# Optimization experiments

Hardware: AMD Instinct MI355X
Metric: run time of the kernel (lower is better)

## Reference

```python
import jax, jax.numpy as jnp
import numpy as np
import math

B, N, L = 1, 256, 384
D_MSA, D_PAIR, H, DH = 256, 128, 8, 32


def layer_norm(x, g, b, eps=1e-5):
    m = jnp.mean(x, axis=-1, keepdims=True)
    v = jnp.var(x, axis=-1, keepdims=True)
    return (x - m) * jax.lax.rsqrt(v + eps) * g + b


def setup_inputs() -> dict:
    key = jax.random.key(0)
    ks = jax.random.split(key, 16)
    hd = H * DH
    w = lambda k, shp, s=0.05: (jax.random.normal(k, shp, dtype=jnp.float32) * s)
    return {
        "msa": jax.random.normal(ks[0], (B, N, L, D_MSA), dtype=jnp.float32),
        "pair": jax.random.normal(ks[1], (B, L, L, D_PAIR), dtype=jnp.float32),
        "ln_msa_g": jnp.ones((D_MSA,), jnp.float32),
        "ln_msa_b": jnp.zeros((D_MSA,), jnp.float32),
        "ln_pair_g": jnp.ones((D_PAIR,), jnp.float32),
        "ln_pair_b": jnp.zeros((D_PAIR,), jnp.float32),
        "sw_q_w": w(ks[2], (D_MSA, hd)),
        "sw_q_b": jnp.zeros((hd,), jnp.float32),
        "sw_k_w": w(ks[3], (D_MSA, hd)),
        "sw_k_b": jnp.zeros((hd,), jnp.float32),
        "wq": w(ks[4], (D_MSA, hd)),
        "wk": w(ks[5], (D_MSA, hd)),
        "wv": w(ks[6], (D_MSA, hd)),
        "wb": w(ks[7], (D_PAIR, H)),
        "wg": w(ks[8], (D_MSA, hd)),
        "bg": jnp.ones((hd,), jnp.float32),
        "wo": w(ks[9], (hd, D_MSA)),
        "bo": jnp.zeros((D_MSA,), jnp.float32),
    }


def reference(msa, pair, ln_msa_g, ln_msa_b, ln_pair_g, ln_pair_b,
              sw_q_w, sw_q_b, sw_k_w, sw_k_b,
              wq, wk, wv, wb, wg, bg, wo, bo):
    b, n, l, _ = msa.shape
    scale = 1.0 / math.sqrt(DH)

    msa_n = layer_norm(msa, ln_msa_g, ln_msa_b)
    pair_n = layer_norm(pair, ln_pair_g, ln_pair_b)

    # SequenceWeight: attention of target seq (row 0) over all N rows, per (L, head)
    tar = msa_n[:, 0]                                       # [B,L,D]
    swq = (tar @ sw_q_w + sw_q_b).reshape(b, l, H, DH) * scale
    swk = (msa_n @ sw_k_w + sw_k_b).reshape(b, n, l, H, DH)
    sw_logits = jnp.einsum('blhd,bnlhd->bnlh', swq, swk)    # [B,N,L,H]
    seq_weight = jax.nn.softmax(sw_logits, axis=1)          # softmax over N (dropout: eval)

    query = (msa_n @ wq).reshape(b, n, l, H, DH) * seq_weight[..., None]
    key = (msa_n @ wk).reshape(b, n, l, H, DH) * scale
    value = (msa_n @ wv).reshape(b, n, l, H, DH)
    bias = pair_n @ wb                                      # [B,L,L,H]
    gate = jax.nn.sigmoid(msa_n @ wg + bg)                  # [B,N,L,H*DH]

    attn = jnp.einsum('bsqhd,bskhd->bqkh', query, key) + bias
    attn = jax.nn.softmax(attn, axis=-2)                    # over k axis
    out = jnp.einsum('bqkh,bskhd->bsqhd', attn, value).reshape(b, n, l, H * DH)
    out = gate * out
    return out @ wo + bo
```

## Files before the change

kernel.cpp:

```cpp
#include <hip/hip_runtime.h>
#include <hip/hip_fp16.h>
#include <stdint.h>

#define NSEQ 256
#define LSEQ 384
#define DM   256
#define DP   128
#define NH   8
#define DHD  32
#define NL   (NSEQ*LSEQ)
#define LL   (LSEQ*LSEQ)
#define SCALE 0.17677669529663687f

typedef unsigned short u16;
typedef short bf16x8 __attribute__((ext_vector_type(8)));
typedef float f32x4 __attribute__((ext_vector_type(4)));

__device__ __forceinline__ float b2f(u16 s){
  union { uint32_t u; float f; } v; v.u = ((uint32_t)s)<<16; return v.f;
}
__device__ __forceinline__ u16 f2b(float f){
  union { float f; uint32_t u; } v; v.f = f;
  uint32_t u = v.u;
  return (u16)((u + 0x7FFFu + ((u>>16)&1u)) >> 16);
}
__device__ __forceinline__ float wsum(float x){
  #pragma unroll
  for(int o=32;o>0;o>>=1) x += __shfl_xor(x,o,64);
  return x;
}
__device__ __forceinline__ float wmax(float x){
  #pragma unroll
  for(int o=32;o>0;o>>=1) x = fmaxf(x, __shfl_xor(x,o,64));
  return x;
}
__device__ __forceinline__ void gload16(const void* g, void* l){
  __builtin_amdgcn_global_load_lds((const __attribute__((address_space(1))) void*)g,
      (__attribute__((address_space(3))) void*)l, 16, 0, 0);
}

__global__ __launch_bounds__(256) void k_ln_msa(const float* __restrict__ msa,
    const float* __restrict__ g, const float* __restrict__ b, u16* __restrict__ out){
  int lane = threadIdx.x & 63;
  int64_t row = (int64_t)blockIdx.x*4 + (threadIdx.x>>6);
  const float4 x = *(const float4*)(msa + row*DM + lane*4);
  float s = x.x+x.y+x.z+x.w;
  float q = x.x*x.x+x.y*x.y+x.z*x.z+x.w*x.w;
  s = wsum(s); q = wsum(q);
  float mean = s*(1.0f/DM);
  float rstd = rsqrtf(q*(1.0f/DM) - mean*mean + 1e-5f);
  int c = lane*4;
  float4 gv = *(const float4*)(g+c);
  float4 bv = *(const float4*)(b+c);
  ushort4 o;
  o.x=f2b((x.x-mean)*rstd*gv.x+bv.x);
  o.y=f2b((x.y-mean)*rstd*gv.y+bv.y);
  o.z=f2b((x.z-mean)*rstd*gv.z+bv.z);
  o.w=f2b((x.w-mean)*rstd*gv.w+bv.w);
  *(ushort4*)(out + row*DM + c) = o;
}

__global__ __launch_bounds__(256) void k_wconv(const float* __restrict__ wq,
    const float* __restrict__ wk, const float* __restrict__ wv,
    const float* __restrict__ wg, const float* __restrict__ wo,
    u16* __restrict__ WTall, u16* __restrict__ WOT){
  __shared__ float tile[64][65];
  int z = blockIdx.z;
  const float* src = (z==0)?wq:(z==1)?wk:(z==2)?wv:(z==3)?wg:wo;
  u16* dst = (z<4) ? (WTall + z*DM*DM) : WOT;
  int k0 = blockIdx.x*64, n0 = blockIdx.y*64, t = threadIdx.x;
  int r = t>>4, c4 = (t&15)*4;
  #pragma unroll
  for(int it=0; it<4; it++){
    float4 v = *(const float4*)(src + (int64_t)(k0 + it*16 + r)*DM + n0 + c4);
    tile[it*16+r][c4+0]=v.x; tile[it*16+r][c4+1]=v.y;
    tile[it*16+r][c4+2]=v.z; tile[it*16+r][c4+3]=v.w;
  }
  __syncthreads();
  #pragma unroll
  for(int it=0; it<4; it++){
    int nl = it*16 + r, kl = c4;
    ushort4 o;
    o.x=f2b(tile[kl+0][nl]); o.y=f2b(tile[kl+1][nl]);
    o.z=f2b(tile[kl+2][nl]); o.w=f2b(tile[kl+3][nl]);
    *(ushort4*)(dst + (int64_t)(n0+nl)*DM + k0 + kl) = o;
  }
}

__global__ __launch_bounds__(256) void k_u(const u16* __restrict__ msa_n,
    const float* __restrict__ sw_q_w, const float* __restrict__ sw_q_b,
    const float* __restrict__ sw_k_w, float* __restrict__ u){
  __shared__ float tar[DM];
  __shared__ float swq[DM];
  int l = blockIdx.x, t = threadIdx.x;
  tar[t] = b2f(msa_n[(int64_t)l*DM + t]);
  __syncthreads();
  float acc = sw_q_b[t];
  for(int c=0;c<DM;c++) acc += tar[c]*sw_q_w[c*DM + t];
  swq[t] = acc * SCALE;
  __syncthreads();
  float res[NH];
  #pragma unroll
  for(int h=0;h<NH;h++){
    float a = 0.f;
    #pragma unroll
    for(int d=0;d<DHD;d+=4){
      float4 w = *(const float4*)(sw_k_w + t*DM + h*DHD + d);
      a += w.x*swq[h*DHD+d] + w.y*swq[h*DHD+d+1] + w.z*swq[h*DHD+d+2] + w.w*swq[h*DHD+d+3];
    }
    res[h]=a;
  }
  #pragma unroll
  for(int h=0;h<NH;h++) u[((int64_t)l*NH + h)*DM + t] = res[h];
}

__global__ __launch_bounds__(256) void k_seqw(const u16* __restrict__ msa_n,
    const float* __restrict__ u, float* __restrict__ sw){
  __shared__ float ul[NH*DM];
  __shared__ float lg[NH*256];
  __shared__ float mx[NH], sm[NH];
  int l = blockIdx.x, t = threadIdx.x;
  #pragma unroll
  for(int h=0;h<NH;h++) ul[h*DM+t] = u[((int64_t)l*NH+h)*DM + t];
  __syncthreads();
  float acc[NH] = {};
  const u16* row = msa_n + ((int64_t)t*LSEQ + l)*DM;
  for(int c=0;c<DM;c+=4){
    ushort4 xv = *(const ushort4*)(row + c);
    float x0=b2f(xv.x), x1=b2f(xv.y), x2=b2f(xv.z), x3=b2f(xv.w);
    #pragma unroll
    for(int h=0;h<NH;h++)
      acc[h] += x0*ul[h*DM+c] + x1*ul[h*DM+c+1] + x2*ul[h*DM+c+2] + x3*ul[h*DM+c+3];
  }
  #pragma unroll
  for(int h=0;h<NH;h++) lg[h*256+t] = acc[h];
  __syncthreads();
  int wv = t>>6, ln = t&63;
  for(int h=wv; h<NH; h+=4){
    float a=lg[h*256+ln], b=lg[h*256+ln+64], c=lg[h*256+ln+128], d=lg[h*256+ln+192];
    float m = wmax(fmaxf(fmaxf(a,b),fmaxf(c,d)));
    float e = __expf(a-m)+__expf(b-m)+__expf(c-m)+__expf(d-m);
    e = wsum(e);
    if(ln==0){ mx[h]=m; sm[h]=1.f/e; }
  }
  __syncthreads();
  float o[NH];
  #pragma unroll
  for(int h=0;h<NH;h++) o[h] = __expf(acc[h]-mx[h])*sm[h];
  float* dst = sw + ((int64_t)t*LSEQ + l)*NH;
  *(float4*)dst     = make_float4(o[0],o[1],o[2],o[3]);
  *(float4*)(dst+4) = make_float4(o[4],o[5],o[6],o[7]);
}

__global__ __launch_bounds__(256) void k_bias(const float* __restrict__ pair,
    const float* __restrict__ g, const float* __restrict__ b,
    const float* __restrict__ wb, float* __restrict__ bias){
  int64_t row = (int64_t)blockIdx.x*256 + threadIdx.x;
  const float* pr = pair + row*DP;
  uint2 xs[32];
  float s = 0.f, q = 0.f;
  #pragma unroll
  for(int i=0;i<32;i++){
    float4 v = *(const float4*)(pr + i*4);
    s += v.x+v.y+v.z+v.w;
    q += v.x*v.x+v.y*v.y+v.z*v.z+v.w*v.w;
    __half2 p0 = __floats2half2_rn(v.x, v.y);
    __half2 p1 = __floats2half2_rn(v.z, v.w);
    xs[i].x = *(const uint32_t*)&p0;
    xs[i].y = *(const uint32_t*)&p1;
  }
  float mean = s*(1.f/DP);
  float rstd = rsqrtf(q*(1.f/DP) - mean*mean + 1e-5f);
  float acc[NH] = {};
  #pragma unroll
  for(int i=0;i<32;i++){
    __half2 p0 = *(const __half2*)&xs[i].x;
    __half2 p1 = *(const __half2*)&xs[i].y;
    float2 f0 = __half22float2(p0);
    float2 f1 = __half22float2(p1);
    float xv[4] = {f0.x, f0.y, f1.x, f1.y};
    #pragma unroll
    for(int c4=0;c4<4;c4++){
      int c = i*4 + c4;
      float y = (xv[c4]-mean)*rstd*g[c] + b[c];
      #pragma unroll
      for(int h=0;h<NH;h++) acc[h] += y*wb[c*NH+h];
    }
  }
  #pragma unroll
  for(int h=0;h<NH;h++) bias[(int64_t)h*LL + row] = acc[h];
}


__global__ __launch_bounds__(256,2) void k_projf(const u16* __restrict__ A,
    const u16* __restrict__ WT, u16* __restrict__ qb, u16* __restrict__ kb,
    u16* __restrict__ gbuf, u16* __restrict__ VT,
    const float* __restrict__ sw, const float* __restrict__ bg){
  __shared__ short As[64*256];
  __shared__ short Bs[128*128];
  int t = threadIdx.x;
  int w = t>>6, lane = t&63, ln15 = lane&15, quad = lane>>4;
  int mw = (w>>1)*32, nw = (w&1)*64;
  int bx = blockIdx.x;
  int64_t r0 = (int64_t)bx*64;

  {
    int rowl = lane>>5;
    int pc = lane&31;
    #pragma unroll
    for(int m=0;m<8;m++){
      int q = w*8+m;
      int row = 2*q + rowl;
      int gch = pc ^ (row&7);
      gload16(A + (r0+row)*DM + gch*8, &As[q*512]);
    }
  }

  for(int nt=0; nt<8; nt++){
    f32x4 acc[4][2] = {};
    #pragma unroll
    for(int kh=0; kh<2; kh++){
      __syncthreads();
      {
        int rowl4 = lane>>4;
        int pc16 = lane&15;
        #pragma unroll
        for(int m=0;m<8;m++){
          int q = w*8+m;
          int row = q*4 + rowl4;
          int gch = pc16 ^ (row&7);
          gload16(WT + (int64_t)(nt*128+row)*DM + kh*128 + gch*8, &Bs[q*512]);
        }
      }
      __syncthreads();
      #pragma unroll
      for(int ks2=0; ks2<4; ks2++){
        bf16x8 af[2], bfv[4];
        #pragma unroll
        for(int i=0;i<2;i++){
          int rw = mw+i*16+ln15;
          int ca = (kh*16 + ks2*4 + quad) ^ (rw&7);
          af[i] = *(const bf16x8*)&As[rw*256 + ca*8];
        }
        #pragma unroll
        for(int j=0;j<4;j++){
          int rw = nw+j*16+ln15;
          int cb = (ks2*4+quad) ^ (rw&7);
          bfv[j] = *(const bf16x8*)&Bs[rw*128 + cb*8];
        }
        #pragma unroll
        for(int j=0;j<4;j++)
          #pragma unroll
          for(int i=0;i<2;i++)
            acc[j][i] = __builtin_amdgcn_mfma_f32_16x16x32_bf16(bfv[j], af[i], acc[j][i], 0,0,0);
      }
    }
    int mode = nt>>1;
    int cmb = (nt&1)*128 + nw;
    if(mode==2){
      int s = bx/6, kpb = (bx%6)*64 + mw;
      #pragma unroll
      for(int j=0;j<4;j++)
        #pragma unroll
        for(int i=0;i<2;i++){
          int kpos = kpb + i*16 + ln15;
          #pragma unroll
          for(int reg=0;reg<4;reg++){
            int cm = cmb + j*16 + quad*4 + reg;
            int hh = cm>>5, d = cm&31;
            VT[((int64_t)(hh*NSEQ+s)*DHD + d)*LSEQ + kpos] = f2b(acc[j][i][reg]);
          }
        }
    } else {
      u16* dst = (mode==0)?qb:(mode==1)?kb:gbuf;
      #pragma unroll
      for(int i=0;i<2;i++){
        int64_t rr = r0 + mw + i*16 + ln15;
        #pragma unroll
        for(int j=0;j<4;j++){
          int cm0 = cmb + j*16 + quad*4;
          ushort4 o;
          #pragma unroll
          for(int reg=0;reg<4;reg++){
            float v = acc[j][i][reg];
            if(mode==0)      v *= sw[rr*NH + ((cm0+reg)>>5)];
            else if(mode==1) v *= SCALE;
            else             v = 1.f/(1.f+__expf(-(v+bg[cm0+reg])));
            ((u16*)&o)[reg] = f2b(v);
          }
          *(ushort4*)(dst + rr*DM + cm0) = o;
        }
      }
    }
  }
}

__global__ __launch_bounds__(256) void k_scores(const u16* __restrict__ Q,
    const u16* __restrict__ K, float* __restrict__ scores){
  __shared__ short As[128*64];
  __shared__ short Bs[128*64];
  int t = threadIdx.x;
  int w = t>>6, lane = t&63, ln15 = lane&15, quad = lane>>4;
  int rIn = lane>>3, cch = lane&7;
  int mw = (w>>1)*64, nw = (w&1)*64;
  int q0 = blockIdx.x*128, k0t = blockIdx.y*128;
  int h = blockIdx.z>>2, sc = blockIdx.z&3;
  int g = cch ^ rIn;
  int s_off = g>>2, d16 = g&3;
  f32x4 acc[4][4] = {};
  for(int i2=0; i2<32; i2++){
    int sb = sc*64 + i2*2 + s_off;
    __syncthreads();
    #pragma unroll
    for(int ti=0; ti<4; ti++){
      int row = w*32 + ti*8 + rIn;
      gload16(Q + ((int64_t)sb*LSEQ + q0 + row)*DM + h*DHD + d16*8, &As[(w*32+ti*8)*64]);
      gload16(K + ((int64_t)sb*LSEQ + k0t + row)*DM + h*DHD + d16*8, &Bs[(w*32+ti*8)*64]);
    }
    __syncthreads();
    #pragma unroll
    for(int kk=0;kk<2;kk++){
      int p = (kk*4+quad) ^ (lane&7);
      bf16x8 af[4], bfv[4];
      #pragma unroll
      for(int i=0;i<4;i++) af[i]  = *(const bf16x8*)&As[(mw+i*16+ln15)*64 + p*8];
      #pragma unroll
      for(int j=0;j<4;j++) bfv[j] = *(const bf16x8*)&Bs[(nw+j*16+ln15)*64 + p*8];
      #pragma unroll
      for(int i=0;i<4;i++)
        #pragma unroll
        for(int j=0;j<4;j++)
          acc[i][j] = __builtin_amdgcn_mfma_f32_16x16x32_bf16(af[i], bfv[j], acc[i][j], 0,0,0);
    }
  }
  int64_t slab = (int64_t)sc*NH*LL;
  #pragma unroll
  for(int i=0;i<4;i++)
    #pragma unroll
    for(int reg=0;reg<4;reg++){
      int q = q0 + mw + i*16 + quad*4 + reg;
      float* rp = scores + slab + ((int64_t)h*LSEQ + q)*LSEQ + k0t + nw + ln15;
      #pragma unroll
      for(int j=0;j<4;j++) rp[j*16] = acc[i][j][reg];
    }
}

__global__ __launch_bounds__(128) void k_softmax(const float* __restrict__ scores,
    const float* __restrict__ bias, u16* __restrict__ Pb){
  int hq = blockIdx.x, t = threadIdx.x;
  int64_t base = (int64_t)hq*LSEQ;
  float v[3];
  #pragma unroll
  for(int i=0;i<3;i++){
    int k = t + i*128;
    float x = bias[base+k];
    x += scores[base+k];
    x += scores[(int64_t)1*NH*LL + base + k];
    x += scores[(int64_t)2*NH*LL + base + k];
    x += scores[(int64_t)3*NH*LL + base + k];
    v[i]=x;
  }
  __shared__ float red[2], red2[2];
  int wv=t>>6, ln=t&63;
  float m = fmaxf(fmaxf(v[0],v[1]),v[2]);
  m = wmax(m);
  if(ln==0) red[wv]=m;
  __syncthreads();
  m = fmaxf(red[0],red[1]);
  float e = __expf(v[0]-m)+__expf(v[1]-m)+__expf(v[2]-m);
  e = wsum(e);
  if(ln==0) red2[wv]=e;
  __syncthreads();
  float inv = 1.f/(red2[0]+red2[1]);
  #pragma unroll
  for(int i=0;i<3;i++) Pb[base + t + i*128] = f2b(__expf(v[i]-m)*inv);
}

__global__ __launch_bounds__(256) void k_pv(const u16* __restrict__ VT,
    const u16* __restrict__ Pb, const u16* __restrict__ gbuf,
    u16* __restrict__ attn){
  __shared__ short As[128*64];
  __shared__ short Bs[128*64];
  int t = threadIdx.x;
  int w = t>>6, lane = t&63, ln15 = lane&15, quad = lane>>4;
  int rIn = lane>>3, cch = lane&7;
  int mw = (w>>1)*64, nw = (w&1)*64;
  int mx = blockIdx.x, ny = blockIdx.y, h = blockIdx.z;
  int g = cch ^ rIn;
  f32x4 acc[4][4] = {};
  for(int it=0; it<6; it++){
    int k0 = it*64;
    __syncthreads();
    #pragma unroll
    for(int ti=0; ti<4; ti++){
      int row = w*32 + ti*8 + rIn;
      gload16(VT + ((int64_t)h*8192 + mx*128 + row)*LSEQ + k0 + g*8, &As[(w*32+ti*8)*64]);
      gload16(Pb + ((int64_t)h*LSEQ + ny*128 + row)*LSEQ + k0 + g*8, &Bs[(w*32+ti*8)*64]);
    }
    __syncthreads();
    #pragma unroll
    for(int kk=0;kk<2;kk++){
      int p = (kk*4+quad) ^ (lane&7);
      bf16x8 af[4], bfv[4];
      #pragma unroll
      for(int i=0;i<4;i++) af[i]  = *(const bf16x8*)&As[(mw+i*16+ln15)*64 + p*8];
      #pragma unroll
      for(int j=0;j<4;j++) bfv[j] = *(const bf16x8*)&Bs[(nw+j*16+ln15)*64 + p*8];
      #pragma unroll
      for(int i=0;i<4;i++)
        #pragma unroll
        for(int j=0;j<4;j++)
          acc[i][j] = __builtin_amdgcn_mfma_f32_16x16x32_bf16(af[i], bfv[j], acc[i][j], 0,0,0);
    }
  }
  #pragma unroll
  for(int i=0;i<4;i++){
    int m0 = mx*128 + mw + i*16 + quad*4;
    int s = m0>>5, d0 = m0&31;
    #pragma unroll
    for(int j=0;j<4;j++){
      int q = ny*128 + nw + j*16 + ln15;
      int64_t base = ((int64_t)s*LSEQ + q)*DM + h*DHD + d0;
      ushort4 gv = *(const ushort4*)(gbuf + base);
      ushort4 o;
      o.x = f2b(acc[i][j][0]*b2f(gv.x));
      o.y = f2b(acc[i][j][1]*b2f(gv.y));
      o.z = f2b(acc[i][j][2]*b2f(gv.z));
      o.w = f2b(acc[i][j][3]*b2f(gv.w));
      *(ushort4*)(attn + base) = o;
    }
  }
}

__global__ __launch_bounds__(256,2) void k_final(const u16* __restrict__ A,
    const u16* __restrict__ WOT, const float* __restrict__ bo,
    float* __restrict__ out){
  __shared__ short As[64*256];
  __shared__ short Bs[128*128];
  int t = threadIdx.x;
  int w = t>>6, lane = t&63, ln15 = lane&15, quad = lane>>4;
  int mw = (w>>1)*32, nw = (w&1)*64;
  int64_t r0 = (int64_t)blockIdx.x*64;

  {
    int rowl = lane>>5;
    int pc = lane&31;
    #pragma unroll
    for(int m=0;m<8;m++){
      int q = w*8+m;
      int row = 2*q + rowl;
      int gch = pc ^ (row&7);
      gload16(A + (r0+row)*DM + gch*8, &As[q*512]);
    }
  }

  for(int nt=0; nt<2; nt++){
    f32x4 acc[4][2] = {};
    #pragma unroll
    for(int kh=0; kh<2; kh++){
      __syncthreads();
      {
        int rowl4 = lane>>4;
        int pc16 = lane&15;
        #pragma unroll
        for(int m=0;m<8;m++){
          int q = w*8+m;
          int row = q*4 + rowl4;
          int gch = pc16 ^ (row&7);
          gload16(WOT + (int64_t)(nt*128+row)*DM + kh*128 + gch*8, &Bs[q*512]);
        }
      }
      __syncthreads();
      #pragma unroll
      for(int ks2=0; ks2<4; ks2++){
        bf16x8 af[2], bfv[4];
        #pragma unroll
        for(int i=0;i<2;i++){
          int rw = mw+i*16+ln15;
          int ca = (kh*16 + ks2*4 + quad) ^ (rw&7);
          af[i] = *(const bf16x8*)&As[rw*256 + ca*8];
        }
        #pragma unroll
        for(int j=0;j<4;j++){
          int rw = nw+j*16+ln15;
          int cb = (ks2*4+quad) ^ (rw&7);
          bfv[j] = *(const bf16x8*)&Bs[rw*128 + cb*8];
        }
        #pragma unroll
        for(int j=0;j<4;j++)
          #pragma unroll
          for(int i=0;i<2;i++)
            acc[j][i] = __builtin_amdgcn_mfma_f32_16x16x32_bf16(bfv[j], af[i], acc[j][i], 0,0,0);
      }
    }
    int n0 = nt*128;
    #pragma unroll
    for(int i=0;i<2;i++){
      int64_t rr = r0 + mw + i*16 + ln15;
      #pragma unroll
      for(int j=0;j<4;j++){
        int cm0 = n0 + nw + j*16 + quad*4;
        float4 o;
        o.x = acc[j][i][0] + bo[cm0+0];
        o.y = acc[j][i][1] + bo[cm0+1];
        o.z = acc[j][i][2] + bo[cm0+2];
        o.w = acc[j][i][3] + bo[cm0+3];
        *(float4*)(out + rr*DM + cm0) = o;
      }
    }
  }
}

extern "C" void kernel_launch(void* const* d_in, const int* in_sizes, int n_in,
                              void* d_out, int out_size, void* d_ws, size_t ws_size,
                              hipStream_t stream){
  const float* msa    = (const float*)d_in[0];
  const float* pair   = (const float*)d_in[1];
  const float* lmg    = (const float*)d_in[2];
  const float* lmb    = (const float*)d_in[3];
  const float* lpg    = (const float*)d_in[4];
  const float* lpb    = (const float*)d_in[5];
  const float* sw_q_w = (const float*)d_in[6];
  const float* sw_q_b = (const float*)d_in[7];
  const float* sw_k_w = (const float*)d_in[8];
  const float* wq     = (const float*)d_in[10];
  const float* wk     = (const float*)d_in[11];
  const float* wv     = (const float*)d_in[12];
  const float* wb     = (const float*)d_in[13];
  const float* wg     = (const float*)d_in[14];
  const float* bg     = (const float*)d_in[15];
  const float* wo     = (const float*)d_in[16];
  const float* bo     = (const float*)d_in[17];
  float* out = (float*)d_out;

  u16* msa_n = (u16*)d_ws;
  u16* qb    = msa_n + (int64_t)NL*DM;
  u16* kb    = qb + (int64_t)NL*DM;
  u16* gbuf  = kb + (int64_t)NL*DM;
  u16* VT    = gbuf + (int64_t)NL*DM;
  u16* Pb    = VT + (int64_t)NL*DM;
  u16* WTall = Pb + (int64_t)NH*LSEQ*LSEQ;
  u16* WOT   = WTall + 1024*DM;
  float* u_buf = (float*)(WOT + DM*DM);
  float* sw  = u_buf + (int64_t)LSEQ*NH*DM;
  float* bias = sw + (int64_t)NL*NH;
  float* scores = bias + (int64_t)NH*LL;
  u16* attnout = msa_n;

  k_ln_msa<<<NL/4, 256, 0, stream>>>(msa, lmg, lmb, msa_n);
  k_wconv<<<dim3(4,4,5), 256, 0, stream>>>(wq, wk, wv, wg, wo, WTall, WOT);
  k_u<<<LSEQ, 256, 0, stream>>>(msa_n, sw_q_w, sw_q_b, sw_k_w, u_buf);
  k_seqw<<<LSEQ, 256, 0, stream>>>(msa_n, u_buf, sw);
  k_bias<<<LL/256, 256, 0, stream>>>(pair, lpg, lpb, wb, bias);
  k_projf<<<dim3(NL/64), 256, 0, stream>>>(msa_n, WTall, qb, kb, gbuf, VT, sw, bg);
  k_scores<<<dim3(3,3,32), 256, 0, stream>>>(qb, kb, scores);
  k_softmax<<<NH*LSEQ, 128, 0, stream>>>(scores, bias, Pb);
  k_pv<<<dim3(64,3,NH), 256, 0, stream>>>(VT, Pb, gbuf, attnout);
  k_final<<<dim3(NL/64), 256, 0, stream>>>(attnout, WOT, bo, out);
}
```

Measured before the change: 683.0 us.

## Double-buffer weight and Q/K tiles in projection, scores, and output GEMMs

The projection, scores, and final GEMM kernels now use two LDS buffers. The next K-slice of weights or Q/K is prefetched while MFMAs run on the current one, and one barrier per step replaces two. The projection kernel also keeps its packed bf16 results in registers and writes them out in batches, using 64-bit stores and vectorised bias loads. This trades higher register pressure, which risks lower occupancy or spills under launch_bounds(256,2), for overlapping global loads with compute.

```diff
diff --git a/kernel.cpp b/kernel.cpp
--- a/kernel.cpp
+++ b/kernel.cpp
@@ -23,6 +23,12 @@
   union { float f; uint32_t u; } v; v.f = f;
   uint32_t u = v.u;
   return (u16)((u + 0x7FFFu + ((u>>16)&1u)) >> 16);
+}
+__device__ __forceinline__ uint2 pack4(float a,float b,float c,float d){
+  uint2 r;
+  r.x = (uint32_t)f2b(a) | ((uint32_t)f2b(b)<<16);
+  r.y = (uint32_t)f2b(c) | ((uint32_t)f2b(d)<<16);
+  return r;
 }
 __device__ __forceinline__ float wsum(float x){
   #pragma unroll
@@ -197,16 +203,17 @@
     u16* __restrict__ gbuf, u16* __restrict__ VT,
     const float* __restrict__ sw, const float* __restrict__ bg){
   __shared__ short As[64*256];
-  __shared__ short Bs[128*128];
+  __shared__ short Bs[2][128*64];
   int t = threadIdx.x;
   int w = t>>6, lane = t&63, ln15 = lane&15, quad = lane>>4;
   int mw = (w>>1)*32, nw = (w&1)*64;
   int bx = blockIdx.x;
   int64_t r0 = (int64_t)bx*64;
+  int rIn = lane>>3, cch = lane&7;
+  int gB = cch ^ rIn;
 
   {
-    int rowl = lane>>5;
-    int pc = lane&31;
+    int rowl = lane>>5, pc = lane&31;
     #pragma unroll
     for(int m=0;m<8;m++){
       int q = w*8+m;
@@ -215,38 +222,46 @@
       gload16(A + (r0+row)*DM + gch*8, &As[q*512]);
     }
   }
-
+  #pragma unroll
+  for(int m=0;m<4;m++){
+    int row = w*32 + m*8 + rIn;
+    gload16(WT + (int64_t)row*DM + gB*8, &Bs[0][(w*32+m*8)*64]);
+  }
+  __syncthreads();
+
+  uint2 rqk[4][2][4];
+  uint2 rvg[4][2][4];
+
+  #pragma unroll
   for(int nt=0; nt<8; nt++){
     f32x4 acc[4][2] = {};
     #pragma unroll
-    for(int kh=0; kh<2; kh++){
-      __syncthreads();
-      {
-        int rowl4 = lane>>4;
-        int pc16 = lane&15;
-        #pragma unroll
-        for(int m=0;m<8;m++){
-          int q = w*8+m;
-          int row = q*4 + rowl4;
-          int gch = pc16 ^ (row&7);
-          gload16(WT + (int64_t)(nt*128+row)*DM + kh*128 + gch*8, &Bs[q*512]);
-        }
-      }
-      __syncthreads();
-      #pragma unroll
-      for(int ks2=0; ks2<4; ks2++){
+    for(int kt=0; kt<4; kt++){
+      int r = nt*4 + kt;
+      int buf = r&1;
+      if(r < 31){
+        int rn = r+1, ntn = rn>>2, ktn = rn&3;
+        #pragma unroll
+        for(int m=0;m<4;m++){
+          int row = w*32 + m*8 + rIn;
+          gload16(WT + (int64_t)(ntn*128+row)*DM + ktn*64 + gB*8,
+                  &Bs[rn&1][(w*32+m*8)*64]);
+        }
+      }
+      #pragma unroll
+      for(int ks2=0; ks2<2; ks2++){
         bf16x8 af[2], bfv[4];
         #pragma unroll
         for(int i=0;i<2;i++){
           int rw = mw+i*16+ln15;
-          int ca = (kh*16 + ks2*4 + quad) ^ (rw&7);
+          int ca = (kt*8 + ks2*4 + quad) ^ (rw&7);
           af[i] = *(const bf16x8*)&As[rw*256 + ca*8];
         }
         #pragma unroll
         for(int j=0;j<4;j++){
           int rw = nw+j*16+ln15;
           int cb = (ks2*4+quad) ^ (rw&7);
-          bfv[j] = *(const bf16x8*)&Bs[rw*128 + cb*8];
+          bfv[j] = *(const bf16x8*)&Bs[buf][rw*64 + cb*8];
         }
         #pragma unroll
         for(int j=0;j<4;j++)
@@ -254,41 +269,85 @@
           for(int i=0;i<2;i++)
             acc[j][i] = __builtin_amdgcn_mfma_f32_16x16x32_bf16(bfv[j], af[i], acc[j][i], 0,0,0);
       }
-    }
-    int mode = nt>>1;
-    int cmb = (nt&1)*128 + nw;
-    if(mode==2){
-      int s = bx/6, kpb = (bx%6)*64 + mw;
-      #pragma unroll
-      for(int j=0;j<4;j++)
+      if(kt==3){
+        int mode = nt>>1;
         #pragma unroll
         for(int i=0;i<2;i++){
-          int kpos = kpb + i*16 + ln15;
+          int64_t rr = r0 + mw + i*16 + ln15;
           #pragma unroll
-          for(int reg=0;reg<4;reg++){
-            int cm = cmb + j*16 + quad*4 + reg;
-            int hh = cm>>5, d = cm&31;
-            VT[((int64_t)(hh*NSEQ+s)*DHD + d)*LSEQ + kpos] = f2b(acc[j][i][reg]);
+          for(int j=0;j<4;j++){
+            int cmn = nw + j*16 + quad*4;
+            float v0=acc[j][i][0], v1=acc[j][i][1], v2=acc[j][i][2], v3=acc[j][i][3];
+            if(mode==0){
+              float s4 = sw[rr*NH + nt*4 + (cmn>>5)];
+              v0*=s4; v1*=s4; v2*=s4; v3*=s4;
+            } else if(mode==1){
+              v0*=SCALE; v1*=SCALE; v2*=SCALE; v3*=SCALE;
+            } else if(mode==3){
+              int cm0 = (nt&1)*128 + cmn;
+              float4 bgv = *(const float4*)(bg + cm0);
+              v0 = 1.f/(1.f+__expf(-(v0+bgv.x)));
+              v1 = 1.f/(1.f+__expf(-(v1+bgv.y)));
+              v2 = 1.f/(1.f+__expf(-(v2+bgv.z)));
+              v3 = 1.f/(1.f+__expf(-(v3+bgv.w)));
+            }
+            if(nt<4) rqk[nt][i][j] = pack4(v0,v1,v2,v3);
+            else     rvg[nt-4][i][j] = pack4(v0,v1,v2,v3);
           }
         }
-    } else {
-      u16* dst = (mode==0)?qb:(mode==1)?kb:gbuf;
+        if(nt==3){
+          #pragma unroll
+          for(int n2=0;n2<4;n2++){
+            u16* dst = (n2<2) ? qb : kb;
+            #pragma unroll
+            for(int i=0;i<2;i++){
+              int64_t rr = r0 + mw + i*16 + ln15;
+              #pragma unroll
+              for(int j=0;j<4;j++){
+                int cm0 = (n2&1)*128 + nw + j*16 + quad*4;
+                *(uint2*)(dst + rr*DM + cm0) = rqk[n2][i][j];
+              }
+            }
+          }
+        }
+      }
+      __syncthreads();
+    }
+  }
+
+  {
+    int s = bx/6, kpb = (bx%6)*64;
+    #pragma unroll
+    for(int n2=0;n2<2;n2++){
+      #pragma unroll
+      for(int i=0;i<2;i++){
+        int kpos = kpb + mw + i*16 + ln15;
+        #pragma unroll
+        for(int j=0;j<4;j++){
+          int cmv = n2*128 + nw + j*16 + quad*4;
+          uint2 pv = rvg[n2][i][j];
+          u16 u0=(u16)(pv.x&0xffff), u1=(u16)(pv.x>>16);
+          u16 u2=(u16)(pv.y&0xffff), u3=(u16)(pv.y>>16);
+          int hh0 = (cmv+0)>>5, d0v = (cmv+0)&31;
+          int hh1 = (cmv+1)>>5, d1v = (cmv+1)&31;
+          int hh2 = (cmv+2)>>5, d2v = (cmv+2)&31;
+          int hh3 = (cmv+3)>>5, d3v = (cmv+3)&31;
+          VT[((int64_t)(hh0*NSEQ+s)*DHD + d0v)*LSEQ + kpos] = u0;
+          VT[((int64_t)(hh1*NSEQ+s)*DHD + d1v)*LSEQ + kpos] = u1;
+          VT[((int64_t)(hh2*NSEQ+s)*DHD + d2v)*LSEQ + kpos] = u2;
+          VT[((int64_t)(hh3*NSEQ+s)*DHD + d3v)*LSEQ + kpos] = u3;
+        }
+      }
+    }
+    #pragma unroll
+    for(int n2=2;n2<4;n2++){
       #pragma unroll
       for(int i=0;i<2;i++){
         int64_t rr = r0 + mw + i*16 + ln15;
         #pragma unroll
         for(int j=0;j<4;j++){
-          int cm0 = cmb + j*16 + quad*4;
-          ushort4 o;
-          #pragma unroll
-          for(int reg=0;reg<4;reg++){
-            float v = acc[j][i][reg];
-            if(mode==0)      v *= sw[rr*NH + ((cm0+reg)>>5)];
-            else if(mode==1) v *= SCALE;
-            else             v = 1.f/(1.f+__expf(-(v+bg[cm0+reg])));
-            ((u16*)&o)[reg] = f2b(v);
-          }
-          *(ushort4*)(dst + rr*DM + cm0) = o;
+          int cm0 = ((n2-2)&1)*128 + nw + j*16 + quad*4;
+          *(uint2*)(gbuf + rr*DM + cm0) = rvg[n2][i][j];
         }
       }
     }
@@ -297,8 +356,8 @@
 
 __global__ __launch_bounds__(256) void k_scores(const u16* __restrict__ Q,
     const u16* __restrict__ K, float* __restrict__ scores){
-  __shared__ short As[128*64];
-  __shared__ short Bs[128*64];
+  __shared__ short As[2][128*64];
+  __shared__ short Bs[2][128*64];
   int t = threadIdx.x;
   int w = t>>6, lane = t&63, ln15 = lane&15, quad = lane>>4;
   int rIn = lane>>3, cch = lane&7;
@@ -307,31 +366,38 @@
   int h = blockIdx.z>>2, sc = blockIdx.z&3;
   int g = cch ^ rIn;
   int s_off = g>>2, d16 = g&3;
-  f32x4 acc[4][4] = {};
-  for(int i2=0; i2<32; i2++){
+
+  auto STAGE = [&](int i2, int bsel){
     int sb = sc*64 + i2*2 + s_off;
-    __syncthreads();
     #pragma unroll
     for(int ti=0; ti<4; ti++){
       int row = w*32 + ti*8 + rIn;
-      gload16(Q + ((int64_t)sb*LSEQ + q0 + row)*DM + h*DHD + d16*8, &As[(w*32+ti*8)*64]);
-      gload16(K + ((int64_t)sb*LSEQ + k0t + row)*DM + h*DHD + d16*8, &Bs[(w*32+ti*8)*64]);
-    }
-    __syncthreads();
+      gload16(Q + ((int64_t)sb*LSEQ + q0 + row)*DM + h*DHD + d16*8, &As[bsel][(w*32+ti*8)*64]);
+      gload16(K + ((int64_t)sb*LSEQ + k0t + row)*DM + h*DHD + d16*8, &Bs[bsel][(w*32+ti*8)*64]);
+    }
+  };
+
+  f32x4 acc[4][4] = {};
+  STAGE(0, 0);
+  __syncthreads();
+  for(int i2=0; i2<32; i2++){
+    int buf = i2&1;
+    if(i2<31) STAGE(i2+1, buf^1);
     #pragma unroll
     for(int kk=0;kk<2;kk++){
       int p = (kk*4+quad) ^ (lane&7);
       bf16x8 af[4], bfv[4];
       #pragma unroll
-      for(int i=0;i<4;i++) af[i]  = *(const bf16x8*)&As[(mw+i*16+ln15)*64 + p*8];
-      #pragma unroll
-      for(int j=0;j<4;j++) bfv[j] = *(const bf16x8*)&Bs[(nw+j*16+ln15)*64 + p*8];
+      for(int i=0;i<4;i++) af[i]  = *(const bf16x8*)&As[buf][(mw+i*16+ln15)*64 + p*8];
+      #pragma unroll
+      for(int j=0;j<4;j++) bfv[j] = *(const bf16x8*)&Bs[buf][(nw+j*16+ln15)*64 + p*8];
       #pragma unroll
       for(int i=0;i<4;i++)
         #pragma unroll
         for(int j=0;j<4;j++)
           acc[i][j] = __builtin_amdgcn_mfma_f32_16x16x32_bf16(af[i], bfv[j], acc[i][j], 0,0,0);
     }
+    __syncthreads();
   }
   int64_t slab = (int64_t)sc*NH*LL;
   #pragma unroll
@@ -436,15 +502,16 @@
     const u16* __restrict__ WOT, const float* __restrict__ bo,
     float* __restrict__ out){
   __shared__ short As[64*256];
-  __shared__ short Bs[128*128];
+  __shared__ short Bs[2][128*64];
   int t = threadIdx.x;
   int w = t>>6, lane = t&63, ln15 = lane&15, quad = lane>>4;
   int mw = (w>>1)*32, nw = (w&1)*64;
   int64_t r0 = (int64_t)blockIdx.x*64;
+  int rIn = lane>>3, cch = lane&7;
+  int gB = cch ^ rIn;
 
   {
-    int rowl = lane>>5;
-    int pc = lane&31;
+    int rowl = lane>>5, pc = lane&31;
     #pragma unroll
     for(int m=0;m<8;m++){
       int q = w*8+m;
@@ -453,38 +520,44 @@
       gload16(A + (r0+row)*DM + gch*8, &As[q*512]);
     }
   }
-
+  #pragma unroll
+  for(int m=0;m<4;m++){
+    int row = w*32 + m*8 + rIn;
+    gload16(WOT + (int64_t)row*DM + gB*8, &Bs[0][(w*32+m*8)*64]);
+  }
+  __syncthreads();
+
+  f32x4 res[2][4][2];
+  #pragma unroll
   for(int nt=0; nt<2; nt++){
     f32x4 acc[4][2] = {};
     #pragma unroll
-    for(int kh=0; kh<2; kh++){
-      __syncthreads();
-      {
-        int rowl4 = lane>>4;
-        int pc16 = lane&15;
-        #pragma unroll
-        for(int m=0;m<8;m++){
-          int q = w*8+m;
-          int row = q*4 + rowl4;
-          int gch = pc16 ^ (row&7);
-          gload16(WOT + (int64_t)(nt*128+row)*DM + kh*128 + gch*8, &Bs[q*512]);
-        }
-      }
-      __syncthreads();
-      #pragma unroll
-      for(int ks2=0; ks2<4; ks2++){
+    for(int kt=0; kt<4; kt++){
+      int r = nt*4 + kt;
+      int buf = r&1;
+      if(r < 7){
+        int rn = r+1, ntn = rn>>2, ktn = rn&3;
+        #pragma unroll
+        for(int m=0;m<4;m++){
+          int row = w*32 + m*8 + rIn;
+          gload16(WOT + (int64_t)(ntn*128+row)*DM + ktn*64 + gB*8,
+                  &Bs[rn&1][(w*32+m*8)*64]);
+        }
+      }
+      #pragma unroll
+      for(int ks2=0; ks2<2; ks2++){
         bf16x8 af[2], bfv[4];
         #pragma unroll
         for(int i=0;i<2;i++){
           int rw = mw+i*16+ln15;
-          int ca = (kh*16 + ks2*4 + quad) ^ (rw&7);
+          int ca = (kt*8 + ks2*4 + quad) ^ (rw&7);
           af[i] = *(const bf16x8*)&As[rw*256 + ca*8];
         }
         #pragma unroll
         for(int j=0;j<4;j++){
           int rw = nw+j*16+ln15;
           int cb = (ks2*4+quad) ^ (rw&7);
-          bfv[j] = *(const bf16x8*)&Bs[rw*128 + cb*8];
+          bfv[j] = *(const bf16x8*)&Bs[buf][rw*64 + cb*8];
         }
         #pragma unroll
         for(int j=0;j<4;j++)
@@ -492,23 +565,31 @@
           for(int i=0;i<2;i++)
             acc[j][i] = __builtin_amdgcn_mfma_f32_16x16x32_bf16(bfv[j], af[i], acc[j][i], 0,0,0);
       }
-    }
-    int n0 = nt*128;
+      __syncthreads();
+    }
+    #pragma unroll
+    for(int j=0;j<4;j++)
+      #pragma unroll
+      for(int i=0;i<2;i++) res[nt][j][i] = acc[j][i];
+  }
+
+  #pragma unroll
+  for(int nt=0; nt<2; nt++)
     #pragma unroll
     for(int i=0;i<2;i++){
       int64_t rr = r0 + mw + i*16 + ln15;
       #pragma unroll
       for(int j=0;j<4;j++){
-        int cm0 = n0 + nw + j*16 + quad*4;
+        int cm0 = nt*128 + nw + j*16 + quad*4;
+        float4 bv = *(const float4*)(bo + cm0);
         float4 o;
-        o.x = acc[j][i][0] + bo[cm0+0];
-        o.y = acc[j][i][1] + bo[cm0+1];
-        o.z = acc[j][i][2] + bo[cm0+2];
-        o.w = acc[j][i][3] + bo[cm0+3];
+        o.x = res[nt][j][i][0] + bv.x;
+        o.y = res[nt][j][i][1] + bv.y;
+        o.z = res[nt][j][i][2] + bv.z;
+        o.w = res[nt][j][i][3] + bv.w;
         *(float4*)(out + rr*DM + cm0) = o;
       }
     }
-  }
 }
 
 extern "C" void kernel_launch(void* const* d_in, const int* in_sizes, int n_in,
```

Result: faster. 662.4 us (-3.0%).
